# Kernel optimization log

Hardware: AMD Instinct MI355X
Metric: run time of the kernel (lower is better)

The kernel has to match this reference:

```python
import jax, jax.numpy as jnp
import numpy as np

B, S, IN, H, D, STATE, PRED = 256, 512, 32, 256, 32, 4, 96


def setup_inputs() -> dict:
    key = jax.random.key(0)
    ks = jax.random.split(key, 16)
    sc = 1.0 / np.sqrt(H)

    def u(k, shape):
        return jax.random.uniform(k, shape, jnp.float32, -sc, sc)

    return {
        "x": jax.random.normal(ks[0], (B, S, IN), jnp.float32),
        # GRU layer 0
        "W_ih_l0": u(ks[1], (3 * H, IN)),
        "W_hh_l0": u(ks[2], (3 * H, H)),
        "b_ih_l0": u(ks[3], (3 * H,)),
        "b_hh_l0": u(ks[4], (3 * H,)),
        # GRU layer 1
        "W_ih_l1": u(ks[5], (3 * H, H)),
        "W_hh_l1": u(ks[6], (3 * H, H)),
        "b_ih_l1": u(ks[7], (3 * H,)),
        "b_hh_l1": u(ks[8], (3 * H,)),
        # state projection: hidden -> STATE*output_dim
        "W_proj": u(ks[9], (STATE * D, H)),
        "b_proj": u(ks[10], (STATE * D,)),
        # observation matrix, eye-initialized (output_dim, STATE)
        "C": jnp.eye(D, STATE, dtype=jnp.float32),
        "raw_level_decay": jnp.zeros((D,), jnp.float32),
        "raw_trend_decay": jnp.zeros((D,), jnp.float32),
        "raw_gamma": jnp.zeros((D,), jnp.float32),
        "omega": jnp.zeros((D,), jnp.float32),
    }


def _gru_layer(xs, W_ih, W_hh, b_ih, b_hh):
    # xs: (B, S, in_dim). Precompute input projections as one big GEMM.
    xp = jnp.einsum('bsi,gi->bsg', xs, W_ih) + b_ih  # (B, S, 3H)

    def step(h, xt):
        gh = h @ W_hh.T + b_hh  # (B, 3H)
        xr, xz, xn = jnp.split(xt, 3, axis=-1)
        hr, hz, hn = jnp.split(gh, 3, axis=-1)
        r = jax.nn.sigmoid(xr + hr)
        z = jax.nn.sigmoid(xz + hz)
        n = jnp.tanh(xn + r * hn)
        h_new = (1.0 - z) * n + z * h
        return h_new, h_new

    h0 = jnp.zeros((xs.shape[0], W_hh.shape[1]), xs.dtype)
    _, hs = jax.lax.scan(step, h0, jnp.swapaxes(xp, 0, 1))  # (S, B, H)
    return jnp.swapaxes(hs, 0, 1)  # (B, S, H)


def reference(x, W_ih_l0, W_hh_l0, b_ih_l0, b_hh_l0,
              W_ih_l1, W_hh_l1, b_ih_l1, b_hh_l1,
              W_proj, b_proj, C,
              raw_level_decay, raw_trend_decay, raw_gamma, omega):
    h1 = _gru_layer(x, W_ih_l0, W_hh_l0, b_ih_l0, b_hh_l0)
    h2 = _gru_layer(h1, W_ih_l1, W_hh_l1, b_ih_l1, b_hh_l1)
    final_h = h2[:, -1, :]  # (B, H)

    d_out = C.shape[0]
    s = (final_h @ W_proj.T + b_proj).reshape(x.shape[0], d_out, STATE)  # (B, D, 4)

    # time-invariant block-diagonal transition coefficients
    a_l = jax.nn.sigmoid(raw_level_decay) * 0.15 + 0.85
    a_t = jax.nn.sigmoid(raw_trend_decay) * 0.25 + 0.7
    g = jax.nn.sigmoid(raw_gamma) * 0.2 + 0.8
    c, sn = jnp.cos(omega), jnp.sin(omega)
    rot00, rot01 = g * c, -g * sn
    rot10, rot11 = g * sn, g * c

    def step(s, _):
        new_s = jnp.stack([
            s[..., 0] * a_l,
            s[..., 1] * a_t,
            s[..., 2] * rot00 + s[..., 3] * rot10,
            s[..., 2] * rot01 + s[..., 3] * rot11,
        ], axis=-1)
        y = jnp.einsum('ds,bds->bd', C, new_s)
        return new_s, y

    _, ys = jax.lax.scan(step, s, None, length=PRED)  # (PRED, B, D)
    return jnp.swapaxes(ys, 0, 1)  # (B, PRED, D)
```

## Files before the change

### kernel.cpp

```cpp
#include <hip/hip_runtime.h>
#include <cstdio>
#include <cstdint>

typedef _Float16 f16;
typedef f16 hf2   __attribute__((ext_vector_type(2)));
typedef f16 f16x8 __attribute__((ext_vector_type(8)));
typedef float f32x4 __attribute__((ext_vector_type(4)));
typedef unsigned int   u32;
typedef unsigned short u16;

#define B_    256
#define S_    512
#define IN_   32
#define H_    256
#define G3_   768
#define D_    32
#define PRED_ 96
#define TC_   32
#define XPAD_ 776

#if __has_builtin(__builtin_amdgcn_fdot2)
__device__ __forceinline__ float fdot2(hf2 a, hf2 b, float c) {
  return __builtin_amdgcn_fdot2(a, b, c, false);
}
#else
__device__ __forceinline__ float fdot2(hf2 a, hf2 b, float c) {
  return c + (float)a[0] * (float)b[0] + (float)a[1] * (float)b[1];
}
#endif

__device__ __forceinline__ float sigm(float x) {
  return __builtin_amdgcn_rcpf(1.f + __expf(-x));
}
__device__ __forceinline__ float tanh_fast(float x) {
  return 1.f - 2.f * __builtin_amdgcn_rcpf(__expf(2.f * x) + 1.f);
}
__device__ __forceinline__ hf2 bc2(u32 v) { return __builtin_bit_cast(hf2, v); }

__global__ void f32_to_f16_k(const float* __restrict__ in, f16* __restrict__ out, int n) {
  int i = blockIdx.x * blockDim.x + threadIdx.x;
  if (i < n) out[i] = (f16)in[i];
}

__device__ __forceinline__ f16x8 cvt8(const float* p) {
  float4 lo = ((const float4*)p)[0];
  float4 hi = ((const float4*)p)[1];
  f16x8 r;
  r[0] = (f16)lo.x; r[1] = (f16)lo.y; r[2] = (f16)lo.z; r[3] = (f16)lo.w;
  r[4] = (f16)hi.x; r[5] = (f16)hi.y; r[6] = (f16)hi.z; r[7] = (f16)hi.w;
  return r;
}

#define ACC4(acc, warr)                       \
  acc = fdot2(warr[cc * 4 + 0], hh0, acc);    \
  acc = fdot2(warr[cc * 4 + 1], hh1, acc);    \
  acc = fdot2(warr[cc * 4 + 2], hh2, acc);    \
  acc = fdot2(warr[cc * 4 + 3], hh3, acc);

template <int LAYER>
__global__ __launch_bounds__(512, 2) void gru_fused(
    const void* __restrict__ Asrc,
    const f16* __restrict__ Wih,
    const float* __restrict__ bih,
    const float* __restrict__ Whh,
    const float* __restrict__ bhh,
    f16* __restrict__ h16_out,
    float* __restrict__ hfinal) {
  constexpr int KK = LAYER ? H_ : IN_;
  const int b   = blockIdx.x;
  const int tid = threadIdx.x;
  const int j2 = tid >> 2, kq = tid & 3;
  const int wv = tid >> 6, lane = tid & 63, lm = lane & 15, q = lane >> 4;

  hf2 w[2][3][32];
#pragma unroll
  for (int jj = 0; jj < 2; jj++) {
    const int j = j2 + jj * 128;
#pragma unroll
    for (int g = 0; g < 3; g++) {
      const float4* src = (const float4*)(Whh + (size_t)(g * 256 + j) * 256 + kq * 64);
#pragma unroll
      for (int u = 0; u < 16; u++) {
        float4 f = src[u];
        w[jj][g][2 * u]     = hf2{(f16)f.x, (f16)f.y};
        w[jj][g][2 * u + 1] = hf2{(f16)f.z, (f16)f.w};
      }
    }
  }
  float bh[2][3];
#pragma unroll
  for (int jj = 0; jj < 2; jj++)
#pragma unroll
    for (int g = 0; g < 3; g++) bh[jj][g] = bhh[g * 256 + j2 + jj * 128];

  __shared__ u16 xpc[TC_ * XPAD_];
  __shared__ __align__(16) u16 h2u[288];
  if (tid < 144) ((u32*)h2u)[tid] = 0u;
  float h[2] = {0.f, 0.f};
  f16* h16p = (LAYER == 0) ? (h16_out + (size_t)b * S_ * H_) : nullptr;

  for (int c = 0; c < S_ / TC_; ++c) {
    const int t0 = c * TC_;
#pragma unroll 1
    for (int nt = 0; nt < 6; ++nt) {
      const int n0 = wv * 96 + nt * 16;
      const f16* Bp = Wih + (size_t)(n0 + lm) * KK + q * 8;
      f32x4 ac0 = {0.f, 0.f, 0.f, 0.f}, ac1 = ac0;
#pragma unroll
      for (int k0 = 0; k0 < KK; k0 += 32) {
        f16x8 bv = *(const f16x8*)(Bp + k0);
        f16x8 a0, a1;
        if constexpr (LAYER == 0) {
          const float* xr = (const float*)Asrc + ((size_t)b * S_ + t0 + lm) * IN_ + k0 + q * 8;
          a0 = cvt8(xr);
          a1 = cvt8(xr + 16 * IN_);
        } else {
          const f16* ar = (const f16*)Asrc + ((size_t)b * S_ + t0 + lm) * H_ + k0 + q * 8;
          a0 = *(const f16x8*)ar;
          a1 = *(const f16x8*)(ar + 16 * H_);
        }
        ac0 = __builtin_amdgcn_mfma_f32_16x16x32_f16(a0, bv, ac0, 0, 0, 0);
        ac1 = __builtin_amdgcn_mfma_f32_16x16x32_f16(a1, bv, ac1, 0, 0, 0);
      }
      const float bb = bih[n0 + lm];
#pragma unroll
      for (int r = 0; r < 4; ++r) {
        xpc[(q * 4 + r) * XPAD_ + n0 + lm]        = __builtin_bit_cast(u16, (f16)(ac0[r] + bb));
        xpc[(16 + q * 4 + r) * XPAD_ + n0 + lm]   = __builtin_bit_cast(u16, (f16)(ac1[r] + bb));
      }
    }
    __syncthreads();

    for (int tl = 0; tl < TC_; ++tl) {
      float ar0 = 0.f, az0 = 0.f, an0 = 0.f, ar1 = 0.f, az1 = 0.f, an1 = 0.f;
      const uint4* hb = (const uint4*)h2u + kq * 9;
#pragma unroll
      for (int cc = 0; cc < 8; ++cc) {
        uint4 hv = hb[cc];
        hf2 hh0 = bc2(hv.x), hh1 = bc2(hv.y), hh2 = bc2(hv.z), hh3 = bc2(hv.w);
        ACC4(ar0, w[0][0]); ACC4(az0, w[0][1]); ACC4(an0, w[0][2]);
        ACC4(ar1, w[1][0]); ACC4(az1, w[1][1]); ACC4(an1, w[1][2]);
      }
      ar0 += __shfl_xor(ar0, 1); ar0 += __shfl_xor(ar0, 2);
      az0 += __shfl_xor(az0, 1); az0 += __shfl_xor(az0, 2);
      an0 += __shfl_xor(an0, 1); an0 += __shfl_xor(an0, 2);
      ar1 += __shfl_xor(ar1, 1); ar1 += __shfl_xor(ar1, 2);
      az1 += __shfl_xor(az1, 1); az1 += __shfl_xor(az1, 2);
      an1 += __shfl_xor(an1, 1); an1 += __shfl_xor(an1, 2);

      const u16* xrow = xpc + tl * XPAD_;
      {
        float xr = (float)__builtin_bit_cast(f16, xrow[j2]);
        float xz = (float)__builtin_bit_cast(f16, xrow[256 + j2]);
        float xn = (float)__builtin_bit_cast(f16, xrow[512 + j2]);
        float r = sigm(xr + ar0 + bh[0][0]);
        float z = sigm(xz + az0 + bh[0][1]);
        float n = tanh_fast(xn + r * (an0 + bh[0][2]));
        h[0] = (1.f - z) * n + z * h[0];
      }
      {
        const int j = j2 + 128;
        float xr = (float)__builtin_bit_cast(f16, xrow[j]);
        float xz = (float)__builtin_bit_cast(f16, xrow[256 + j]);
        float xn = (float)__builtin_bit_cast(f16, xrow[512 + j]);
        float r = sigm(xr + ar1 + bh[1][0]);
        float z = sigm(xz + az1 + bh[1][1]);
        float n = tanh_fast(xn + r * (an1 + bh[1][2]));
        h[1] = (1.f - z) * n + z * h[1];
      }
      __syncthreads();
      if (kq == 0) {
        h2u[(j2 >> 6) * 72 + (j2 & 63)] = __builtin_bit_cast(u16, (f16)h[0]);
        if constexpr (LAYER == 0) h16p[(size_t)(t0 + tl) * H_ + j2] = (f16)h[0];
      } else if (kq == 1) {
        const int jb = j2 + 128;
        h2u[(jb >> 6) * 72 + (jb & 63)] = __builtin_bit_cast(u16, (f16)h[1]);
        if constexpr (LAYER == 0) h16p[(size_t)(t0 + tl) * H_ + jb] = (f16)h[1];
      }
      __syncthreads();
    }
  }
  if constexpr (LAYER == 1) {
    if (kq == 0)      hfinal[b * H_ + j2]       = h[0];
    else if (kq == 1) hfinal[b * H_ + 128 + j2] = h[1];
  }
}

__global__ __launch_bounds__(128) void proj_rollout(
    const float* __restrict__ hfinal, const float* __restrict__ Wp,
    const float* __restrict__ bp, const float* __restrict__ Cm,
    const float* __restrict__ rld, const float* __restrict__ rtd,
    const float* __restrict__ rg, const float* __restrict__ om,
    float* __restrict__ out) {
  const int b = blockIdx.x, tid = threadIdx.x;
  __shared__ float fh[256];
  __shared__ float sb[128];
  ((float2*)fh)[tid] = ((const float2*)(hfinal + b * 256))[tid];
  __syncthreads();
  const float4* wrow = (const float4*)(Wp + tid * 256);
  float acc = 0.f;
#pragma unroll 16
  for (int k4 = 0; k4 < 64; k4++) {
    float4 wv = wrow[k4];
    acc += wv.x * fh[4 * k4] + wv.y * fh[4 * k4 + 1] + wv.z * fh[4 * k4 + 2] +
           wv.w * fh[4 * k4 + 3];
  }
  sb[tid] = acc + bp[tid];
  __syncthreads();
  if (tid < 32) {
    const int dd = tid;
    float s0 = sb[dd * 4], s1 = sb[dd * 4 + 1], s2 = sb[dd * 4 + 2], s3 = sb[dd * 4 + 3];
    float al = sigm(rld[dd]) * 0.15f + 0.85f;
    float at = sigm(rtd[dd]) * 0.25f + 0.70f;
    float g  = sigm(rg[dd]) * 0.20f + 0.80f;
    float cw = cosf(om[dd]), sw = sinf(om[dd]);
    float r00 = g * cw, r01 = -g * sw, r10 = g * sw, r11 = g * cw;
    float c0 = Cm[dd * 4], c1 = Cm[dd * 4 + 1], c2 = Cm[dd * 4 + 2], c3 = Cm[dd * 4 + 3];
    float* op = out + (size_t)b * PRED_ * D_ + dd;
    for (int t = 0; t < PRED_; t++) {
      float n0 = s0 * al, n1 = s1 * at;
      float n2 = s2 * r00 + s3 * r10;
      float n3 = s2 * r01 + s3 * r11;
      op[(size_t)t * D_] = c0 * n0 + c1 * n1 + c2 * n2 + c3 * n3;
      s0 = n0; s1 = n1; s2 = n2; s3 = n3;
    }
  }
}

extern "C" void kernel_launch(void* const* d_in, const int* in_sizes, int n_in,
                              void* d_out, int out_size, void* d_ws,
                              size_t ws_size, hipStream_t stream) {
  (void)in_sizes; (void)n_in; (void)out_size;
  const float* x     = (const float*)d_in[0];
  const float* Wih0  = (const float*)d_in[1];
  const float* Whh0  = (const float*)d_in[2];
  const float* bih0  = (const float*)d_in[3];
  const float* bhh0  = (const float*)d_in[4];
  const float* Wih1  = (const float*)d_in[5];
  const float* Whh1  = (const float*)d_in[6];
  const float* bih1  = (const float*)d_in[7];
  const float* bhh1  = (const float*)d_in[8];
  const float* Wproj = (const float*)d_in[9];
  const float* bproj = (const float*)d_in[10];
  const float* Cm    = (const float*)d_in[11];
  const float* rld   = (const float*)d_in[12];
  const float* rtd   = (const float*)d_in[13];
  const float* rg    = (const float*)d_in[14];
  const float* om    = (const float*)d_in[15];
  float* out = (float*)d_out;

  char* ws = (char*)d_ws;
  const size_t wi0_off = 0;
  const size_t wi1_off = 49152;
  const size_t h16_off = 442368;
  const size_t hf_off  = 67551232;
  const size_t need    = 67813376;
  if (ws_size < need) {
    fprintf(stderr, "kernel_launch: ws too small: have %zu need %zu — skipping\n",
            ws_size, need);
    return;
  }
  f16* wi016  = (f16*)(ws + wi0_off);
  f16* wi116  = (f16*)(ws + wi1_off);
  f16* h16    = (f16*)(ws + h16_off);
  float* hfin = (float*)(ws + hf_off);

  f32_to_f16_k<<<96, 256, 0, stream>>>(Wih0, wi016, G3_ * IN_);
  f32_to_f16_k<<<768, 256, 0, stream>>>(Wih1, wi116, G3_ * H_);
  gru_fused<0><<<B_, 512, 0, stream>>>((const void*)x,   wi016, bih0, Whh0, bhh0, h16, nullptr);
  gru_fused<1><<<B_, 512, 0, stream>>>((const void*)h16, wi116, bih1, Whh1, bhh1, nullptr, hfin);
  proj_rollout<<<B_, 128, 0, stream>>>(hfin, Wproj, bproj, Cm, rld, rtd, rg, om, out);
}
```

Before: 1.830 ms.

## Repartition GRU recurrence to one unit per thread pair with double-buffered hidden state

Each thread pair now owns one hidden unit and splits the K dimension in halves, instead of four threads splitting K across two units. The reduction drops to a single shuffle. The hidden vector is double-buffered in shared memory, which removes one of the two barriers per timestep. The fdot2 chains use two accumulators to shorten dependency chains. Launch bounds move to one block per SM, leaving more registers for the 192 half2 weights per thread, at the cost of lower occupancy.

```diff
diff --git a/kernel.cpp b/kernel.cpp
--- a/kernel.cpp
+++ b/kernel.cpp
@@ -51,14 +51,8 @@
   return r;
 }
 
-#define ACC4(acc, warr)                       \
-  acc = fdot2(warr[cc * 4 + 0], hh0, acc);    \
-  acc = fdot2(warr[cc * 4 + 1], hh1, acc);    \
-  acc = fdot2(warr[cc * 4 + 2], hh2, acc);    \
-  acc = fdot2(warr[cc * 4 + 3], hh3, acc);
-
 template <int LAYER>
-__global__ __launch_bounds__(512, 2) void gru_fused(
+__global__ __launch_bounds__(512, 1) void gru_fused(
     const void* __restrict__ Asrc,
     const f16* __restrict__ Wih,
     const float* __restrict__ bih,
@@ -69,35 +63,30 @@
   constexpr int KK = LAYER ? H_ : IN_;
   const int b   = blockIdx.x;
   const int tid = threadIdx.x;
-  const int j2 = tid >> 2, kq = tid & 3;
+  const int p  = tid >> 1, kh = tid & 1;
   const int wv = tid >> 6, lane = tid & 63, lm = lane & 15, q = lane >> 4;
 
-  hf2 w[2][3][32];
-#pragma unroll
-  for (int jj = 0; jj < 2; jj++) {
-    const int j = j2 + jj * 128;
-#pragma unroll
-    for (int g = 0; g < 3; g++) {
-      const float4* src = (const float4*)(Whh + (size_t)(g * 256 + j) * 256 + kq * 64);
-#pragma unroll
-      for (int u = 0; u < 16; u++) {
-        float4 f = src[u];
-        w[jj][g][2 * u]     = hf2{(f16)f.x, (f16)f.y};
-        w[jj][g][2 * u + 1] = hf2{(f16)f.z, (f16)f.w};
-      }
-    }
-  }
-  float bh[2][3];
-#pragma unroll
-  for (int jj = 0; jj < 2; jj++)
-#pragma unroll
-    for (int g = 0; g < 3; g++) bh[jj][g] = bhh[g * 256 + j2 + jj * 128];
+  hf2 w[3][64];
+#pragma unroll
+  for (int g = 0; g < 3; g++) {
+    const float4* src = (const float4*)(Whh + (size_t)(g * 256 + p) * 256 + kh * 128);
+#pragma unroll
+    for (int u = 0; u < 32; u++) {
+      float4 f = src[u];
+      w[g][2 * u]     = hf2{(f16)f.x, (f16)f.y};
+      w[g][2 * u + 1] = hf2{(f16)f.z, (f16)f.w};
+    }
+  }
+  float bh[3];
+#pragma unroll
+  for (int g = 0; g < 3; g++) bh[g] = bhh[g * 256 + p];
 
   __shared__ u16 xpc[TC_ * XPAD_];
-  __shared__ __align__(16) u16 h2u[288];
-  if (tid < 144) ((u32*)h2u)[tid] = 0u;
-  float h[2] = {0.f, 0.f};
+  __shared__ __align__(16) u16 hbuf[2][256];
+  if (tid < 128) ((u32*)hbuf[0])[tid] = 0u;
+  float h = 0.f;
   f16* h16p = (LAYER == 0) ? (h16_out + (size_t)b * S_ * H_) : nullptr;
+  int cur = 0;
 
   for (int c = 0; c < S_ / TC_; ++c) {
     const int t0 = c * TC_;
@@ -125,64 +114,56 @@
       const float bb = bih[n0 + lm];
 #pragma unroll
       for (int r = 0; r < 4; ++r) {
-        xpc[(q * 4 + r) * XPAD_ + n0 + lm]        = __builtin_bit_cast(u16, (f16)(ac0[r] + bb));
-        xpc[(16 + q * 4 + r) * XPAD_ + n0 + lm]   = __builtin_bit_cast(u16, (f16)(ac1[r] + bb));
+        xpc[(q * 4 + r) * XPAD_ + n0 + lm]      = __builtin_bit_cast(u16, (f16)(ac0[r] + bb));
+        xpc[(16 + q * 4 + r) * XPAD_ + n0 + lm] = __builtin_bit_cast(u16, (f16)(ac1[r] + bb));
       }
     }
     __syncthreads();
 
     for (int tl = 0; tl < TC_; ++tl) {
-      float ar0 = 0.f, az0 = 0.f, an0 = 0.f, ar1 = 0.f, az1 = 0.f, an1 = 0.f;
-      const uint4* hb = (const uint4*)h2u + kq * 9;
-#pragma unroll
-      for (int cc = 0; cc < 8; ++cc) {
+      float ar = 0.f, az = 0.f, an = 0.f, ar2 = 0.f, az2 = 0.f, an2 = 0.f;
+      const uint4* hb = (const uint4*)hbuf[cur] + kh * 16;
+#pragma unroll
+      for (int cc = 0; cc < 16; ++cc) {
         uint4 hv = hb[cc];
-        hf2 hh0 = bc2(hv.x), hh1 = bc2(hv.y), hh2 = bc2(hv.z), hh3 = bc2(hv.w);
-        ACC4(ar0, w[0][0]); ACC4(az0, w[0][1]); ACC4(an0, w[0][2]);
-        ACC4(ar1, w[1][0]); ACC4(az1, w[1][1]); ACC4(an1, w[1][2]);
-      }
-      ar0 += __shfl_xor(ar0, 1); ar0 += __shfl_xor(ar0, 2);
-      az0 += __shfl_xor(az0, 1); az0 += __shfl_xor(az0, 2);
-      an0 += __shfl_xor(an0, 1); an0 += __shfl_xor(an0, 2);
-      ar1 += __shfl_xor(ar1, 1); ar1 += __shfl_xor(ar1, 2);
-      az1 += __shfl_xor(az1, 1); az1 += __shfl_xor(az1, 2);
-      an1 += __shfl_xor(an1, 1); an1 += __shfl_xor(an1, 2);
+        hf2 h0 = bc2(hv.x), h1 = bc2(hv.y), h2v = bc2(hv.z), h3 = bc2(hv.w);
+        ar  = fdot2(w[0][4 * cc],     h0,  ar);
+        ar2 = fdot2(w[0][4 * cc + 1], h1,  ar2);
+        ar  = fdot2(w[0][4 * cc + 2], h2v, ar);
+        ar2 = fdot2(w[0][4 * cc + 3], h3,  ar2);
+        az  = fdot2(w[1][4 * cc],     h0,  az);
+        az2 = fdot2(w[1][4 * cc + 1], h1,  az2);
+        az  = fdot2(w[1][4 * cc + 2], h2v, az);
+        az2 = fdot2(w[1][4 * cc + 3], h3,  az2);
+        an  = fdot2(w[2][4 * cc],     h0,  an);
+        an2 = fdot2(w[2][4 * cc + 1], h1,  an2);
+        an  = fdot2(w[2][4 * cc + 2], h2v, an);
+        an2 = fdot2(w[2][4 * cc + 3], h3,  an2);
+      }
+      ar += ar2; az += az2; an += an2;
+      ar += __shfl_xor(ar, 1);
+      az += __shfl_xor(az, 1);
+      an += __shfl_xor(an, 1);
 
       const u16* xrow = xpc + tl * XPAD_;
-      {
-        float xr = (float)__builtin_bit_cast(f16, xrow[j2]);
-        float xz = (float)__builtin_bit_cast(f16, xrow[256 + j2]);
-        float xn = (float)__builtin_bit_cast(f16, xrow[512 + j2]);
-        float r = sigm(xr + ar0 + bh[0][0]);
-        float z = sigm(xz + az0 + bh[0][1]);
-        float n = tanh_fast(xn + r * (an0 + bh[0][2]));
-        h[0] = (1.f - z) * n + z * h[0];
-      }
-      {
-        const int j = j2 + 128;
-        float xr = (float)__builtin_bit_cast(f16, xrow[j]);
-        float xz = (float)__builtin_bit_cast(f16, xrow[256 + j]);
-        float xn = (float)__builtin_bit_cast(f16, xrow[512 + j]);
-        float r = sigm(xr + ar1 + bh[1][0]);
-        float z = sigm(xz + az1 + bh[1][1]);
-        float n = tanh_fast(xn + r * (an1 + bh[1][2]));
-        h[1] = (1.f - z) * n + z * h[1];
+      float xr = (float)__builtin_bit_cast(f16, xrow[p]);
+      float xz = (float)__builtin_bit_cast(f16, xrow[256 + p]);
+      float xn = (float)__builtin_bit_cast(f16, xrow[512 + p]);
+      float r = sigm(xr + ar + bh[0]);
+      float z = sigm(xz + az + bh[1]);
+      float n = tanh_fast(xn + r * (an + bh[2]));
+      h = (1.f - z) * n + z * h;
+
+      if (kh == 0) {
+        hbuf[cur ^ 1][p] = __builtin_bit_cast(u16, (f16)h);
+        if constexpr (LAYER == 0) h16p[(size_t)(t0 + tl) * H_ + p] = (f16)h;
       }
       __syncthreads();
-      if (kq == 0) {
-        h2u[(j2 >> 6) * 72 + (j2 & 63)] = __builtin_bit_cast(u16, (f16)h[0]);
-        if constexpr (LAYER == 0) h16p[(size_t)(t0 + tl) * H_ + j2] = (f16)h[0];
-      } else if (kq == 1) {
-        const int jb = j2 + 128;
-        h2u[(jb >> 6) * 72 + (jb & 63)] = __builtin_bit_cast(u16, (f16)h[1]);
-        if constexpr (LAYER == 0) h16p[(size_t)(t0 + tl) * H_ + jb] = (f16)h[1];
-      }
-      __syncthreads();
+      cur ^= 1;
     }
   }
   if constexpr (LAYER == 1) {
-    if (kq == 0)      hfinal[b * H_ + j2]       = h[0];
-    else if (kq == 1) hfinal[b * H_ + 128 + j2] = h[1];
+    if (kh == 0) hfinal[b * H_ + p] = h;
   }
 }
 
```

Result: faster. 1.599 ms (-12.6%).
